# Kernel optimization log

Measured on AMD Instinct MI355X. Metric: run time of the kernel, lower is better.

The kernel has to match this reference:

```python
import jax, jax.numpy as jnp
import numpy as np

N, C, K2 = 40000, 128, 9  # active voxels, channels, 3x3 kernel taps
HEAD_OUT = {"hm": 3, "center": 2, "center_z": 1, "dim": 3, "rot": 2}
EPS = 1e-5
INIT_BIAS = -2.66


def setup_inputs() -> dict:
    key = jax.random.key(0)
    ks = jax.random.split(key, 16)
    feats = jax.random.normal(ks[0], (N, C), dtype=jnp.float32)
    # precomputed submanifold-conv neighbor indices (one per kernel tap, all valid)
    nbr_idx = jax.random.randint(ks[1], (N, K2), 0, N, dtype=jnp.int32)
    H = len(HEAD_OUT)
    inp = {"feats": feats, "nbr_idx": nbr_idx}
    # stacked 3x3 SubMConv weights for all heads (kaiming-ish scale)
    inp["W1"] = jax.random.normal(ks[2], (H, K2, C, C), dtype=jnp.float32) * (2.0 / (K2 * C)) ** 0.5
    inp["gamma"] = jnp.ones((H, C), jnp.float32)
    inp["beta"] = jnp.zeros((H, C), jnp.float32)
    for i, (name, oc) in enumerate(HEAD_OUT.items()):
        inp[f"w_{name}"] = jax.random.normal(ks[3 + i], (C, oc), dtype=jnp.float32) * (2.0 / C) ** 0.5
        inp[f"b_{name}"] = (jnp.full((oc,), INIT_BIAS, jnp.float32) if name == "hm"
                             else jnp.zeros((oc,), jnp.float32))
    return inp


def reference(feats, nbr_idx, W1, gamma, beta,
              w_hm, b_hm, w_center, b_center, w_center_z, b_center_z,
              w_dim, b_dim, w_rot, b_rot):
    # SubMConv2d as gather + contraction over kernel taps (shared by all heads)
    gathered = feats[nbr_idx]                       # [N, K2, C]
    y = jnp.einsum('nkc,hkcd->hnd', gathered, W1)   # [H, N, C]
    # BatchNorm1d (training-mode forward: biased batch stats over voxels) + ReLU
    mean = y.mean(axis=1, keepdims=True)
    var = y.var(axis=1, keepdims=True)
    y = jax.nn.relu((y - mean) * jax.lax.rsqrt(var + EPS) * gamma[:, None, :] + beta[:, None, :])
    # per-head 1x1 SubMConv with bias
    heads = [(w_hm, b_hm), (w_center, b_center), (w_center_z, b_center_z),
             (w_dim, b_dim), (w_rot, b_rot)]
    outs = [y[i] @ w + b for i, (w, b) in enumerate(heads)]
    # concat head outputs along channel: [N, 3+2+1+3+2] = [N, 11]
    return jnp.concatenate(outs, axis=-1)
```

## Files before the change

kernel.cpp:

```cpp
#include <hip/hip_runtime.h>
#include <stdint.h>

#define NVOX 40000
#define CCH  128
#define K2   9
#define NH   5
#define TILES 313

typedef __attribute__((ext_vector_type(8))) short bf16x8;
typedef __attribute__((ext_vector_type(4))) float f32x4;

__device__ __forceinline__ unsigned short f2b(float f) {
  union { float f; unsigned int u; } v; v.f = f;
  return (unsigned short)((v.u + 0x7fffu + ((v.u >> 16) & 1u)) >> 16);
}
__device__ __forceinline__ float b2f(unsigned short u) {
  union { unsigned int u; float f; } v; v.u = ((unsigned int)u) << 16;
  return v.f;
}
__device__ __forceinline__ void g2l16(const void* g, void* l) {
  __builtin_amdgcn_global_load_lds(
      (const __attribute__((address_space(1))) unsigned int*)g,
      (__attribute__((address_space(3))) unsigned int*)l, 16, 0, 0);
}
__device__ __forceinline__ int swz(int row, int col) {
  return row * 128 + ((((col >> 3) ^ (row & 15)) << 3) | (col & 7));
}

__global__ void prep(const float4* __restrict__ feats, ushort4* __restrict__ fb,
                     const float* __restrict__ w1, unsigned short* __restrict__ w1t,
                     float* __restrict__ sums) {
  __shared__ unsigned short t[64 * 34];
  int b = blockIdx.x;
  if (b < 5000) {
    int i = b * 256 + threadIdx.x;
    if (i < NVOX * CCH / 4) {
      float4 v = feats[i];
      ushort4 r;
      r.x = f2b(v.x); r.y = f2b(v.y); r.z = f2b(v.z); r.w = f2b(v.w);
      fb[i] = r;
    }
    return;
  }
  if (b == 5360) {
    for (int i = threadIdx.x; i < 2 * NH * CCH; i += 256) sums[i] = 0.f;
    return;
  }
  int bb = b - 5000;
  int tile = bb >> 3;
  int q = (bb >> 1) & 3;
  int dh = bb & 1;
  const float* src = w1 + (size_t)tile * 16384 + q * 32 * 128 + dh * 64;
  for (int e = threadIdx.x; e < 2048; e += 256) {
    int c = e >> 6, dd = e & 63;
    t[dd * 34 + c] = f2b(src[c * 128 + dd]);
  }
  __syncthreads();
  unsigned short* dst = w1t + (size_t)tile * 16384 + q * 32;
  for (int e = threadIdx.x; e < 2048; e += 256) {
    int d = e >> 5, c = e & 31;
    dst[(dh * 64 + d) * 128 + c] = t[d * 34 + c];
  }
}

__device__ __forceinline__ void stageBhalf8(unsigned short* dst, const unsigned short* wp,
                                            int half, int wave, int lane) {
  int lrow = lane >> 3;
  int lch  = lane & 7;
#pragma unroll
  for (int i = 0; i < 2; ++i) {
    int blk = wave * 2 + i;
    g2l16(wp + (blk * 8 + lrow) * 128 + half * 64 + ((lch ^ lrow) << 3),
          &dst[blk * 512]);
  }
}

__global__ void __launch_bounds__(512, 4) conv_gemm(
    const unsigned short* __restrict__ fb,
    const int* __restrict__ nbr,
    const unsigned short* __restrict__ w1t,
    unsigned short* __restrict__ yb,
    float* __restrict__ sums)
{
  __shared__ __align__(16) unsigned short Bsb[2][64 * 128];
  __shared__ int idxs[128 * K2];

  const int bid = blockIdx.x;
  const int s = bid / 40;
  const int r = bid % 40;
  const int h = r >> 3;
  const int x = r & 7;
  const int tile = s * 8 + x;
  if (tile >= TILES) return;
  const int n0 = tile * 128;

  const int tid = threadIdx.x;
  const int wave = tid >> 6;
  const int lane = tid & 63;
  const int m = lane & 15;
  const int quad = lane >> 4;

  const unsigned short* wh = w1t + ((size_t)h * K2 << 14);

  stageBhalf8(Bsb[0], wh, 0, wave, lane);

  for (int i = tid; i < 128 * K2; i += 512) {
    int rr = i / K2;
    int gn = n0 + rr; if (gn > NVOX - 1) gn = NVOX - 1;
    idxs[i] = nbr[gn * K2 + (i - rr * K2)];
  }
  __syncthreads();

  bf16x8 A[2][4];
  {
    int i0 = idxs[(wave * 16 + m) * K2 + 0];
    const unsigned short* p0 = fb + (size_t)i0 * CCH + quad * 8;
#pragma unroll
    for (int kc = 0; kc < 4; ++kc)
      A[0][kc] = *(const bf16x8*)(p0 + kc * 32);
  }
  asm volatile("s_waitcnt vmcnt(0)" ::: "memory");
  __syncthreads();

  f32x4 acc[8] = {};

#pragma unroll
  for (int k = 0; k < K2; ++k) {
    const int par = k & 1;

    stageBhalf8(Bsb[1], wh + ((size_t)k << 14), 1, wave, lane);
    if (k + 1 < K2) {
      int i0 = idxs[(wave * 16 + m) * K2 + k + 1];
      const unsigned short* p0 = fb + (size_t)i0 * CCH + quad * 8;
#pragma unroll
      for (int kc = 0; kc < 4; ++kc)
        A[par ^ 1][kc] = *(const bf16x8*)(p0 + kc * 32);
    }
#pragma unroll
    for (int kc = 0; kc < 2; ++kc) {
      bf16x8 bfr[8];
#pragma unroll
      for (int ni = 0; ni < 8; ++ni)
        bfr[ni] = *(const bf16x8*)&Bsb[0][(ni * 16 + m) * 64 + ((((kc & 1) * 4 + quad) ^ (m & 7)) << 3)];
#pragma unroll
      for (int ni = 0; ni < 8; ++ni)
        acc[ni] = __builtin_amdgcn_mfma_f32_16x16x32_bf16(A[par][kc], bfr[ni], acc[ni], 0, 0, 0);
    }
    asm volatile("s_waitcnt vmcnt(0)" ::: "memory");
    __syncthreads();

    if (k + 1 < K2)
      stageBhalf8(Bsb[0], wh + ((size_t)(k + 1) << 14), 0, wave, lane);
#pragma unroll
    for (int kc = 2; kc < 4; ++kc) {
      bf16x8 bfr[8];
#pragma unroll
      for (int ni = 0; ni < 8; ++ni)
        bfr[ni] = *(const bf16x8*)&Bsb[1][(ni * 16 + m) * 64 + ((((kc & 1) * 4 + quad) ^ (m & 7)) << 3)];
#pragma unroll
      for (int ni = 0; ni < 8; ++ni)
        acc[ni] = __builtin_amdgcn_mfma_f32_16x16x32_bf16(A[par][kc], bfr[ni], acc[ni], 0, 0, 0);
    }
    asm volatile("s_waitcnt vmcnt(0)" ::: "memory");
    __syncthreads();
  }

  const bool full = (n0 + 128 <= NVOX);
  unsigned short* epi = &Bsb[0][0];

#pragma unroll
  for (int ni = 0; ni < 8; ++ni)
#pragma unroll
    for (int rr = 0; rr < 4; ++rr) {
      int row = wave * 16 + quad * 4 + rr;
      int col = ni * 16 + m;
      epi[swz(row, col)] = f2b(acc[ni][rr]);
    }

  float psm[8], pq[8];
#pragma unroll
  for (int ni = 0; ni < 8; ++ni) {
    float sm = 0.f, q = 0.f;
#pragma unroll
    for (int rr = 0; rr < 4; ++rr) {
      float v = acc[ni][rr];
      if (!full && n0 + wave * 16 + quad * 4 + rr >= NVOX) v = 0.f;
      sm += v; q += v * v;
    }
    sm += __shfl_xor(sm, 16); q += __shfl_xor(q, 16);
    sm += __shfl_xor(sm, 32); q += __shfl_xor(q, 32);
    psm[ni] = sm; pq[ni] = q;
  }
  __syncthreads();

  for (int i = tid; i < 2048; i += 512) {
    int row = i >> 4;
    int c = i & 15;
    if (n0 + row < NVOX)
      *(bf16x8*)(yb + ((size_t)h * NVOX + n0 + row) * CCH + c * 8) =
          *(const bf16x8*)&epi[row * 128 + ((c ^ (row & 15)) << 3)];
  }
  __syncthreads();

  float2* pb = (float2*)&Bsb[0][0];
  if (quad == 0)
#pragma unroll
    for (int ni = 0; ni < 8; ++ni)
      pb[(ni * 16 + m) * 9 + wave] = make_float2(psm[ni], pq[ni]);
  __syncthreads();

  if (tid < 128) {
    float sm = 0.f, q = 0.f;
#pragma unroll
    for (int c = 0; c < 8; ++c) {
      float2 p = pb[tid * 9 + c];
      sm += p.x; q += p.y;
    }
    atomicAdd(&sums[h * CCH + tid], sm);
    atomicAdd(&sums[NH * CCH + h * CCH + tid], q);
  }
}

__global__ void __launch_bounds__(256) head_fuse(
    const unsigned short* __restrict__ yb, const float* __restrict__ sums,
    const float* __restrict__ gamma, const float* __restrict__ beta,
    const float* __restrict__ w_hm, const float* __restrict__ b_hm,
    const float* __restrict__ w_ce, const float* __restrict__ b_ce,
    const float* __restrict__ w_cz, const float* __restrict__ b_cz,
    const float* __restrict__ w_dm, const float* __restrict__ b_dm,
    const float* __restrict__ w_rt, const float* __restrict__ b_rt,
    float* __restrict__ out)
{
  __shared__ unsigned short t[64 * 128];
  __shared__ float pbuf[4][64][12];
  __shared__ float scl[NH * CCH], shf[NH * CCH];

  const int tid = threadIdx.x;
  const int v0 = blockIdx.x * 64;
  const int vx = tid & 63;
  const int qd = tid >> 6;

  for (int i = tid; i < NH * CCH; i += 256) {
    float mean = sums[i] * (1.f / NVOX);
    float var = sums[NH * CCH + i] * (1.f / NVOX) - mean * mean;
    float rstd = rsqrtf(var + 1e-5f);
    float sc = rstd * gamma[i];
    scl[i] = sc;
    shf[i] = beta[i] - mean * sc;
  }

  float part[11];
#pragma unroll
  for (int j = 0; j < 11; ++j) part[j] = 0.f;

#pragma unroll
  for (int h = 0; h < NH; ++h) {
    __syncthreads();
#pragma unroll
    for (int i = 0; i < 4; ++i) {
      int idx = i * 256 + tid;
      int row = idx >> 4, c = idx & 15;
      *(bf16x8*)&t[row * 128 + ((c ^ (row & 15)) << 3)] =
          *(const bf16x8*)(yb + ((size_t)h * NVOX + v0 + row) * CCH + c * 8);
    }
    __syncthreads();

    const float* sc = scl + h * CCH;
    const float* sh = shf + h * CCH;
    const float* wp; int oc, off;
    switch (h) {
      case 0: wp = w_hm; oc = 3; off = 0; break;
      case 1: wp = w_ce; oc = 2; off = 3; break;
      case 2: wp = w_cz; oc = 1; off = 5; break;
      case 3: wp = w_dm; oc = 3; off = 6; break;
      default: wp = w_rt; oc = 2; off = 9; break;
    }
#pragma unroll
    for (int qq = 0; qq < 4; ++qq) {
      int q8 = qd * 4 + qq;
      bf16x8 pk = *(const bf16x8*)&t[vx * 128 + ((q8 ^ (vx & 15)) << 3)];
#pragma unroll
      for (int e = 0; e < 8; ++e) {
        int d = q8 * 8 + e;
        float z = fmaf(b2f((unsigned short)pk[e]), sc[d], sh[d]);
        z = fmaxf(z, 0.f);
        const float* wr = wp + d * oc;
        part[off] = fmaf(z, wr[0], part[off]);
        if (oc > 1) part[off + 1] = fmaf(z, wr[1], part[off + 1]);
        if (oc > 2) part[off + 2] = fmaf(z, wr[2], part[off + 2]);
      }
    }
  }

#pragma unroll
  for (int j = 0; j < 11; ++j) pbuf[qd][vx][j] = part[j];
  __syncthreads();
  if (tid < 64) {
    float o[11];
#pragma unroll
    for (int j = 0; j < 11; ++j)
      o[j] = pbuf[0][tid][j] + pbuf[1][tid][j] + pbuf[2][tid][j] + pbuf[3][tid][j];
    o[0] += b_hm[0]; o[1] += b_hm[1]; o[2] += b_hm[2];
    o[3] += b_ce[0]; o[4] += b_ce[1];
    o[5] += b_cz[0];
    o[6] += b_dm[0]; o[7] += b_dm[1]; o[8] += b_dm[2];
    o[9] += b_rt[0]; o[10] += b_rt[1];
    float* op = out + (size_t)(v0 + tid) * 11;
#pragma unroll
    for (int j = 0; j < 11; ++j) op[j] = o[j];
  }
}

extern "C" void kernel_launch(void* const* d_in, const int* in_sizes, int n_in,
                              void* d_out, int out_size, void* d_ws, size_t ws_size,
                              hipStream_t stream) {
  const float* feats = (const float*)d_in[0];
  const int*   nbr   = (const int*)d_in[1];
  const float* W1    = (const float*)d_in[2];
  const float* gamma = (const float*)d_in[3];
  const float* beta  = (const float*)d_in[4];
  const float* w_hm = (const float*)d_in[5];  const float* b_hm = (const float*)d_in[6];
  const float* w_ce = (const float*)d_in[7];  const float* b_ce = (const float*)d_in[8];
  const float* w_cz = (const float*)d_in[9];  const float* b_cz = (const float*)d_in[10];
  const float* w_dm = (const float*)d_in[11]; const float* b_dm = (const float*)d_in[12];
  const float* w_rt = (const float*)d_in[13]; const float* b_rt = (const float*)d_in[14];
  float* out = (float*)d_out;

  char* ws = (char*)d_ws;
  unsigned short* w1t = (unsigned short*)ws;
  unsigned short* fb  = (unsigned short*)(ws + 11796480);
  unsigned short* yb  = (unsigned short*)(ws + 22036480);
  float* sums = (float*)(ws + 73236480);

  prep<<<5361, 256, 0, stream>>>((const float4*)feats, (ushort4*)fb, W1, w1t, sums);
  conv_gemm<<<1600, 512, 0, stream>>>(fb, nbr, w1t, yb, sums);
  head_fuse<<<625, 256, 0, stream>>>(yb, sums, gamma, beta, w_hm, b_hm, w_ce, b_ce,
                                     w_cz, b_cz, w_dm, b_dm, w_rt, b_rt, out);
}
```

Before: 241.3 us.

## Triple-buffer weight stages, 2x2 wave tiling in conv GEMM, split head_fuse per head

```diff
diff --git a/kernel.cpp b/kernel.cpp
--- a/kernel.cpp
+++ b/kernel.cpp
@@ -63,14 +63,14 @@
   }
 }
 
-__device__ __forceinline__ void stageBhalf8(unsigned short* dst, const unsigned short* wp,
+__device__ __forceinline__ void stageBhalf8(unsigned short* dst, const unsigned short* wp_tap,
                                             int half, int wave, int lane) {
   int lrow = lane >> 3;
   int lch  = lane & 7;
 #pragma unroll
   for (int i = 0; i < 2; ++i) {
     int blk = wave * 2 + i;
-    g2l16(wp + (blk * 8 + lrow) * 128 + half * 64 + ((lch ^ lrow) << 3),
+    g2l16(wp_tap + (blk * 8 + lrow) * 128 + half * 64 + ((lch ^ lrow) << 3),
           &dst[blk * 512]);
   }
 }
@@ -82,7 +82,7 @@
     unsigned short* __restrict__ yb,
     float* __restrict__ sums)
 {
-  __shared__ __align__(16) unsigned short Bsb[2][64 * 128];
+  __shared__ __align__(16) unsigned short Bsb[3][64 * 128];
   __shared__ int idxs[128 * K2];
 
   const int bid = blockIdx.x;
@@ -99,10 +99,10 @@
   const int lane = tid & 63;
   const int m = lane & 15;
   const int quad = lane >> 4;
+  const int wr = wave >> 1;
+  const int wc = wave & 1;
 
   const unsigned short* wh = w1t + ((size_t)h * K2 << 14);
-
-  stageBhalf8(Bsb[0], wh, 0, wave, lane);
 
   for (int i = tid; i < 128 * K2; i += 512) {
     int rr = i / K2;
@@ -111,87 +111,106 @@
   }
   __syncthreads();
 
-  bf16x8 A[2][4];
+  bf16x8 A[2][2][2];
+
+  stageBhalf8(Bsb[0], wh, 0, wave, lane);
   {
-    int i0 = idxs[(wave * 16 + m) * K2 + 0];
+    int i0 = idxs[(wr * 32 + m) * K2 + 0];
+    int i1 = idxs[(wr * 32 + 16 + m) * K2 + 0];
     const unsigned short* p0 = fb + (size_t)i0 * CCH + quad * 8;
-#pragma unroll
-    for (int kc = 0; kc < 4; ++kc)
-      A[0][kc] = *(const bf16x8*)(p0 + kc * 32);
-  }
-  asm volatile("s_waitcnt vmcnt(0)" ::: "memory");
-  __syncthreads();
-
-  f32x4 acc[8] = {};
-
-#pragma unroll
-  for (int k = 0; k < K2; ++k) {
-    const int par = k & 1;
-
-    stageBhalf8(Bsb[1], wh + ((size_t)k << 14), 1, wave, lane);
-    if (k + 1 < K2) {
-      int i0 = idxs[(wave * 16 + m) * K2 + k + 1];
-      const unsigned short* p0 = fb + (size_t)i0 * CCH + quad * 8;
-#pragma unroll
-      for (int kc = 0; kc < 4; ++kc)
-        A[par ^ 1][kc] = *(const bf16x8*)(p0 + kc * 32);
-    }
-#pragma unroll
-    for (int kc = 0; kc < 2; ++kc) {
-      bf16x8 bfr[8];
-#pragma unroll
-      for (int ni = 0; ni < 8; ++ni)
-        bfr[ni] = *(const bf16x8*)&Bsb[0][(ni * 16 + m) * 64 + ((((kc & 1) * 4 + quad) ^ (m & 7)) << 3)];
-#pragma unroll
-      for (int ni = 0; ni < 8; ++ni)
-        acc[ni] = __builtin_amdgcn_mfma_f32_16x16x32_bf16(A[par][kc], bfr[ni], acc[ni], 0, 0, 0);
-    }
-    asm volatile("s_waitcnt vmcnt(0)" ::: "memory");
-    __syncthreads();
-
-    if (k + 1 < K2)
-      stageBhalf8(Bsb[0], wh + ((size_t)(k + 1) << 14), 0, wave, lane);
-#pragma unroll
-    for (int kc = 2; kc < 4; ++kc) {
-      bf16x8 bfr[8];
-#pragma unroll
-      for (int ni = 0; ni < 8; ++ni)
-        bfr[ni] = *(const bf16x8*)&Bsb[1][(ni * 16 + m) * 64 + ((((kc & 1) * 4 + quad) ^ (m & 7)) << 3)];
-#pragma unroll
-      for (int ni = 0; ni < 8; ++ni)
-        acc[ni] = __builtin_amdgcn_mfma_f32_16x16x32_bf16(A[par][kc], bfr[ni], acc[ni], 0, 0, 0);
-    }
-    asm volatile("s_waitcnt vmcnt(0)" ::: "memory");
-    __syncthreads();
+    const unsigned short* p1 = fb + (size_t)i1 * CCH + quad * 8;
+    A[0][0][0] = *(const bf16x8*)(p0);
+    A[0][0][1] = *(const bf16x8*)(p0 + 32);
+    A[0][1][0] = *(const bf16x8*)(p1);
+    A[0][1][1] = *(const bf16x8*)(p1 + 32);
+  }
+  stageBhalf8(Bsb[1], wh, 1, wave, lane);
+  asm volatile("s_waitcnt vmcnt(2)" ::: "memory");
+  __builtin_amdgcn_s_barrier();
+
+  f32x4 acc[2][4] = {};
+
+#pragma unroll
+  for (int p = 0; p < 18; ++p) {
+    const int par = p & 1;
+
+    if (p < 17) {
+      int tn = (p + 1) >> 1, kp = (p + 1) & 1;
+      int i0 = idxs[(wr * 32 + m) * K2 + tn];
+      int i1 = idxs[(wr * 32 + 16 + m) * K2 + tn];
+      const unsigned short* p0 = fb + (size_t)i0 * CCH + kp * 64 + quad * 8;
+      const unsigned short* p1 = fb + (size_t)i1 * CCH + kp * 64 + quad * 8;
+      A[par ^ 1][0][0] = *(const bf16x8*)(p0);
+      A[par ^ 1][0][1] = *(const bf16x8*)(p0 + 32);
+      A[par ^ 1][1][0] = *(const bf16x8*)(p1);
+      A[par ^ 1][1][1] = *(const bf16x8*)(p1 + 32);
+    }
+    if (p < 16)
+      stageBhalf8(Bsb[(p + 2) % 3], wh + ((size_t)((p + 2) >> 1) << 14),
+                  (p + 2) & 1, wave, lane);
+
+    const unsigned short* Bcur = Bsb[p % 3];
+#pragma unroll
+    for (int kcL = 0; kcL < 2; ++kcL) {
+      bf16x8 bfr[4];
+#pragma unroll
+      for (int nj = 0; nj < 4; ++nj) {
+        int row = wc * 64 + nj * 16 + m;
+        bfr[nj] = *(const bf16x8*)&Bcur[row * 64 + (((kcL * 4 + quad) ^ (m & 7)) << 3)];
+      }
+#pragma unroll
+      for (int nj = 0; nj < 4; ++nj) {
+        acc[0][nj] = __builtin_amdgcn_mfma_f32_16x16x32_bf16(A[par][0][kcL], bfr[nj], acc[0][nj], 0, 0, 0);
+        acc[1][nj] = __builtin_amdgcn_mfma_f32_16x16x32_bf16(A[par][1][kcL], bfr[nj], acc[1][nj], 0, 0, 0);
+      }
+    }
+
+    if (p < 16) {
+      asm volatile("s_waitcnt vmcnt(2)" ::: "memory");
+      __builtin_amdgcn_s_barrier();
+    } else if (p == 16) {
+      asm volatile("s_waitcnt vmcnt(0)" ::: "memory");
+      __builtin_amdgcn_s_barrier();
+    }
   }
 
   const bool full = (n0 + 128 <= NVOX);
   unsigned short* epi = &Bsb[0][0];
 
 #pragma unroll
-  for (int ni = 0; ni < 8; ++ni)
-#pragma unroll
-    for (int rr = 0; rr < 4; ++rr) {
-      int row = wave * 16 + quad * 4 + rr;
-      int col = ni * 16 + m;
-      epi[swz(row, col)] = f2b(acc[ni][rr]);
-    }
-
-  float psm[8], pq[8];
-#pragma unroll
-  for (int ni = 0; ni < 8; ++ni) {
+  for (int mi = 0; mi < 2; ++mi)
+#pragma unroll
+    for (int nj = 0; nj < 4; ++nj)
+#pragma unroll
+      for (int rr = 0; rr < 4; ++rr) {
+        int row = wr * 32 + mi * 16 + quad * 4 + rr;
+        int col = wc * 64 + nj * 16 + m;
+        epi[swz(row, col)] = f2b(acc[mi][nj][rr]);
+      }
+
+  float psm[4], pq[4];
+#pragma unroll
+  for (int nj = 0; nj < 4; ++nj) {
     float sm = 0.f, q = 0.f;
 #pragma unroll
-    for (int rr = 0; rr < 4; ++rr) {
-      float v = acc[ni][rr];
-      if (!full && n0 + wave * 16 + quad * 4 + rr >= NVOX) v = 0.f;
-      sm += v; q += v * v;
-    }
+    for (int mi = 0; mi < 2; ++mi)
+#pragma unroll
+      for (int rr = 0; rr < 4; ++rr) {
+        float v = acc[mi][nj][rr];
+        if (!full && n0 + wr * 32 + mi * 16 + quad * 4 + rr >= NVOX) v = 0.f;
+        sm += v; q += v * v;
+      }
     sm += __shfl_xor(sm, 16); q += __shfl_xor(q, 16);
     sm += __shfl_xor(sm, 32); q += __shfl_xor(q, 32);
-    psm[ni] = sm; pq[ni] = q;
-  }
-  __syncthreads();
+    psm[nj] = sm; pq[nj] = q;
+  }
+  __syncthreads();
+
+  float2* pb = (float2*)&Bsb[2][0];
+  if (quad == 0)
+#pragma unroll
+    for (int nj = 0; nj < 4; ++nj)
+      pb[(wc * 64 + nj * 16 + m) * 5 + wr] = make_float2(psm[nj], pq[nj]);
 
   for (int i = tid; i < 2048; i += 512) {
     int row = i >> 4;
@@ -202,19 +221,12 @@
   }
   __syncthreads();
 
-  float2* pb = (float2*)&Bsb[0][0];
-  if (quad == 0)
-#pragma unroll
-    for (int ni = 0; ni < 8; ++ni)
-      pb[(ni * 16 + m) * 9 + wave] = make_float2(psm[ni], pq[ni]);
-  __syncthreads();
-
   if (tid < 128) {
     float sm = 0.f, q = 0.f;
 #pragma unroll
-    for (int c = 0; c < 8; ++c) {
-      float2 p = pb[tid * 9 + c];
-      sm += p.x; q += p.y;
+    for (int c = 0; c < 4; ++c) {
+      float2 pv = pb[tid * 5 + c];
+      sm += pv.x; q += pv.y;
     }
     atomicAdd(&sums[h * CCH + tid], sm);
     atomicAdd(&sums[NH * CCH + h * CCH + tid], q);
@@ -232,82 +244,69 @@
     float* __restrict__ out)
 {
   __shared__ unsigned short t[64 * 128];
-  __shared__ float pbuf[4][64][12];
-  __shared__ float scl[NH * CCH], shf[NH * CCH];
+  __shared__ float pbuf[4][64][3];
+  __shared__ float scl[CCH], shf[CCH];
 
   const int tid = threadIdx.x;
-  const int v0 = blockIdx.x * 64;
+  const int h  = blockIdx.x % NH;
+  const int v0 = (blockIdx.x / NH) * 64;
   const int vx = tid & 63;
   const int qd = tid >> 6;
 
-  for (int i = tid; i < NH * CCH; i += 256) {
+  const float* wp; const float* bp; int oc, off;
+  switch (h) {
+    case 0: wp = w_hm; bp = b_hm; oc = 3; off = 0; break;
+    case 1: wp = w_ce; bp = b_ce; oc = 2; off = 3; break;
+    case 2: wp = w_cz; bp = b_cz; oc = 1; off = 5; break;
+    case 3: wp = w_dm; bp = b_dm; oc = 3; off = 6; break;
+    default: wp = w_rt; bp = b_rt; oc = 2; off = 9; break;
+  }
+
+  if (tid < CCH) {
+    int i = h * CCH + tid;
     float mean = sums[i] * (1.f / NVOX);
     float var = sums[NH * CCH + i] * (1.f / NVOX) - mean * mean;
     float rstd = rsqrtf(var + 1e-5f);
     float sc = rstd * gamma[i];
-    scl[i] = sc;
-    shf[i] = beta[i] - mean * sc;
-  }
-
-  float part[11];
-#pragma unroll
-  for (int j = 0; j < 11; ++j) part[j] = 0.f;
-
-#pragma unroll
-  for (int h = 0; h < NH; ++h) {
-    __syncthreads();
-#pragma unroll
-    for (int i = 0; i < 4; ++i) {
-      int idx = i * 256 + tid;
-      int row = idx >> 4, c = idx & 15;
-      *(bf16x8*)&t[row * 128 + ((c ^ (row & 15)) << 3)] =
-          *(const bf16x8*)(yb + ((size_t)h * NVOX + v0 + row) * CCH + c * 8);
-    }
-    __syncthreads();
-
-    const float* sc = scl + h * CCH;
-    const float* sh = shf + h * CCH;
-    const float* wp; int oc, off;
-    switch (h) {
-      case 0: wp = w_hm; oc = 3; off = 0; break;
-      case 1: wp = w_ce; oc = 2; off = 3; break;
-      case 2: wp = w_cz; oc = 1; off = 5; break;
-      case 3: wp = w_dm; oc = 3; off = 6; break;
-      default: wp = w_rt; oc = 2; off = 9; break;
-    }
-#pragma unroll
-    for (int qq = 0; qq < 4; ++qq) {
-      int q8 = qd * 4 + qq;
-      bf16x8 pk = *(const bf16x8*)&t[vx * 128 + ((q8 ^ (vx & 15)) << 3)];
-#pragma unroll
-      for (int e = 0; e < 8; ++e) {
-        int d = q8 * 8 + e;
-        float z = fmaf(b2f((unsigned short)pk[e]), sc[d], sh[d]);
-        z = fmaxf(z, 0.f);
-        const float* wr = wp + d * oc;
-        part[off] = fmaf(z, wr[0], part[off]);
-        if (oc > 1) part[off + 1] = fmaf(z, wr[1], part[off + 1]);
-        if (oc > 2) part[off + 2] = fmaf(z, wr[2], part[off + 2]);
-      }
-    }
-  }
-
-#pragma unroll
-  for (int j = 0; j < 11; ++j) pbuf[qd][vx][j] = part[j];
-  __syncthreads();
+    scl[tid] = sc;
+    shf[tid] = beta[i] - mean * sc;
+  }
+#pragma unroll
+  for (int i = 0; i < 4; ++i) {
+    int idx = i * 256 + tid;
+    int row = idx >> 4, c = idx & 15;
+    *(bf16x8*)&t[row * 128 + ((c ^ (row & 15)) << 3)] =
+        *(const bf16x8*)(yb + ((size_t)h * NVOX + v0 + row) * CCH + c * 8);
+  }
+  __syncthreads();
+
+  float p0 = 0.f, p1 = 0.f, p2 = 0.f;
+#pragma unroll
+  for (int qq = 0; qq < 4; ++qq) {
+    int q8 = qd * 4 + qq;
+    bf16x8 pk = *(const bf16x8*)&t[vx * 128 + ((q8 ^ (vx & 15)) << 3)];
+#pragma unroll
+    for (int e = 0; e < 8; ++e) {
+      int d = q8 * 8 + e;
+      float z = fmaf(b2f((unsigned short)pk[e]), scl[d], shf[d]);
+      z = fmaxf(z, 0.f);
+      const float* wr = wp + d * oc;
+      p0 = fmaf(z, wr[0], p0);
+      if (oc > 1) p1 = fmaf(z, wr[1], p1);
+      if (oc > 2) p2 = fmaf(z, wr[2], p2);
+    }
+  }
+  pbuf[qd][vx][0] = p0;
+  if (oc > 1) pbuf[qd][vx][1] = p1;
+  if (oc > 2) pbuf[qd][vx][2] = p2;
+  __syncthreads();
+
   if (tid < 64) {
-    float o[11];
-#pragma unroll
-    for (int j = 0; j < 11; ++j)
-      o[j] = pbuf[0][tid][j] + pbuf[1][tid][j] + pbuf[2][tid][j] + pbuf[3][tid][j];
-    o[0] += b_hm[0]; o[1] += b_hm[1]; o[2] += b_hm[2];
-    o[3] += b_ce[0]; o[4] += b_ce[1];
-    o[5] += b_cz[0];
-    o[6] += b_dm[0]; o[7] += b_dm[1]; o[8] += b_dm[2];
-    o[9] += b_rt[0]; o[10] += b_rt[1];
-    float* op = out + (size_t)(v0 + tid) * 11;
-#pragma unroll
-    for (int j = 0; j < 11; ++j) op[j] = o[j];
+    float* op = out + (size_t)(v0 + tid) * 11 + off;
+#pragma unroll
+    for (int j = 0; j < 3; ++j)
+      if (j < oc)
+        op[j] = bp[j] + pbuf[0][tid][j] + pbuf[1][tid][j] + pbuf[2][tid][j] + pbuf[3][tid][j];
   }
 }
 
@@ -334,6 +333,6 @@
 
   prep<<<5361, 256, 0, stream>>>((const float4*)feats, (ushort4*)fb, W1, w1t, sums);
   conv_gemm<<<1600, 512, 0, stream>>>(fb, nbr, w1t, yb, sums);
-  head_fuse<<<625, 256, 0, stream>>>(yb, sums, gamma, beta, w_hm, b_hm, w_ce, b_ce,
-                                     w_cz, b_cz, w_dm, b_dm, w_rt, b_rt, out);
-}
+  head_fuse<<<3125, 256, 0, stream>>>(yb, sums, gamma, beta, w_hm, b_hm, w_ce, b_ce,
+                                      w_cz, b_cz, w_dm, b_dm, w_rt, b_rt, out);
+}
```

Result: slower. 270.8 us (+12.2%).
